# Kernel optimization log

Measured on AMD Instinct MI355X. Metric: run time of the kernel, lower is better.

Reference implementation:

```python
import jax, jax.numpy as jnp
import numpy as np

B, S, D, H, L = 64, 512, 1024, 1024, 2


def setup_inputs() -> dict:
    key = jax.random.key(0)
    ks = jax.random.split(key, 5)
    scale = 1.0 / np.sqrt(D + H)  # ~torch Linear init scale
    return {
        "x": jax.random.normal(ks[0], (B, S, D), dtype=jnp.float32),
        "W_r": jax.random.normal(ks[1], (L, D + H, H), dtype=jnp.float32) * scale,
        "W_z": jax.random.normal(ks[2], (L, D + H, H), dtype=jnp.float32) * scale,
        "W_h": jax.random.normal(ks[3], (L, D + H, H), dtype=jnp.float32) * scale,
        "b_r": jnp.zeros((L, H), dtype=jnp.float32),
        "b_z": jnp.zeros((L, H), dtype=jnp.float32),
        "b_h": jnp.zeros((L, H), dtype=jnp.float32),
    }


def _gru_layer(x_seq, Wr, Wz, Wh, br, bz, bh):
    # x_seq: [S, B, D]; returns [S, B, H]
    h0 = jnp.zeros((x_seq.shape[1], Wr.shape[1]), dtype=x_seq.dtype)

    def step(h, xt):
        xh = jnp.concatenate([xt, h], axis=-1)          # [B, D+H]
        r = jax.nn.sigmoid(xh @ Wr + br)
        z = jax.nn.sigmoid(xh @ Wz + bz)
        xrh = jnp.concatenate([xt, r * h], axis=-1)
        n = jnp.tanh(xrh @ Wh + bh)
        h_new = (1.0 - z) * n + z * h
        return h_new, h_new

    _, ys = jax.lax.scan(step, h0, x_seq)
    return ys


def reference(x, W_r, W_z, W_h, b_r, b_z, b_h):
    seq = jnp.swapaxes(x, 0, 1)  # [S, B, D]
    for i in range(W_r.shape[0]):
        seq = _gru_layer(seq, W_r[i], W_z[i], W_h[i], b_r[i], b_z[i], b_h[i])
    return jnp.swapaxes(seq, 0, 1)  # [B, S, H]
```

## Files before the change

kernel.cpp:

```cpp
#include <hip/hip_runtime.h>


#define TPB 256
#define NBLK 256
#define B_ 64
#define S_ 512
#define H_ 1024
#define KTOT 2048
#define NROW 32768

typedef float f32x4 __attribute__((ext_vector_type(4)));
typedef short short8 __attribute__((ext_vector_type(8)));

#define WX_HI  0
#define WX_LO  12288
#define WRZ_HI 24576
#define WRZ_LO 32768
#define WN_HI  40960
#define WN_LO  45056
#define A_HI   49152
#define A_LO   65536
#define LDS_SHORTS 81920

#define MFMA16 __builtin_amdgcn_mfma_f32_16x16x32_bf16

#define GLL(gp, lp) \
    __builtin_amdgcn_global_load_lds((__attribute__((address_space(1))) const void*)(const void*)(gp), \
                                     (__attribute__((address_space(3))) void*)(void*)(lp), 16, 0, 0x11)

__device__ __forceinline__ unsigned short f2bf(float f) {
    unsigned u = __float_as_uint(f);
    u += 0x7fffu + ((u >> 16) & 1u);
    return (unsigned short)(u >> 16);
}
__device__ __forceinline__ float bf2f(unsigned short s) {
    return __uint_as_float(((unsigned)s) << 16);
}
__device__ __forceinline__ float sigm(float v) { return 1.0f / (1.0f + expf(-v)); }

__device__ __forceinline__ void store_short_bypass(const unsigned short* addr, unsigned short v) {
    asm volatile("global_store_short %0, %1, off sc0 sc1"
                 :: "v"((unsigned long long)(uintptr_t)addr), "v"((unsigned)v) : "memory");
}
__device__ __forceinline__ void waitcnt0() {
    asm volatile("s_waitcnt vmcnt(0)" ::: "memory");
}

__device__ __forceinline__ void gbar(unsigned* bar, int grp) {
    __syncthreads();
    if (threadIdx.x == 0) {
        unsigned* cnt  = bar + grp * 32;
        unsigned* gen  = bar + 256 + grp * 32;
        unsigned* ccnt = bar + 512;
        unsigned g = __hip_atomic_load(gen, __ATOMIC_RELAXED, __HIP_MEMORY_SCOPE_AGENT);
        if (__hip_atomic_fetch_add(cnt, 1u, __ATOMIC_RELAXED, __HIP_MEMORY_SCOPE_AGENT) == 31u) {
            __hip_atomic_store(cnt, 0u, __ATOMIC_RELAXED, __HIP_MEMORY_SCOPE_AGENT);
            waitcnt0();
            if (__hip_atomic_fetch_add(ccnt, 1u, __ATOMIC_RELAXED, __HIP_MEMORY_SCOPE_AGENT) == 7u) {
                __hip_atomic_store(ccnt, 0u, __ATOMIC_RELAXED, __HIP_MEMORY_SCOPE_AGENT);
                waitcnt0();
                #pragma unroll
                for (int i = 0; i < 8; ++i)
                    __hip_atomic_store(bar + 256 + i * 32, g + 1u,
                                       __ATOMIC_RELAXED, __HIP_MEMORY_SCOPE_AGENT);
            } else {
                while (__hip_atomic_load(gen, __ATOMIC_RELAXED, __HIP_MEMORY_SCOPE_AGENT) == g)
                    __builtin_amdgcn_s_sleep(8);
            }
        } else {
            while (__hip_atomic_load(gen, __ATOMIC_RELAXED, __HIP_MEMORY_SCOPE_AGENT) == g)
                __builtin_amdgcn_s_sleep(8);
        }
    }
    __syncthreads();
}

__global__ __launch_bounds__(TPB, 1) void gru_fk(
    const float* __restrict__ x,
    const float* __restrict__ Wr,
    const float* __restrict__ Wz,
    const float* __restrict__ Wh,
    const float* __restrict__ pbr,
    const float* __restrict__ pbz,
    const float* __restrict__ pbh,
    float* __restrict__ out,
    unsigned short* __restrict__ h_hi,
    unsigned short* __restrict__ h_lo,
    unsigned short* __restrict__ rh_hi,
    unsigned short* __restrict__ rh_lo,
    float* __restrict__ hpriv,
    float* __restrict__ zpriv,
    unsigned short* __restrict__ xs_hi,
    unsigned short* __restrict__ xs_lo,
    unsigned* __restrict__ bar)
{
    __shared__ short lds[LDS_SHORTS];
    const int lane = threadIdx.x & 63;
    const int wave = threadIdx.x >> 6;
    const int c0   = blockIdx.x << 2;
    const int grp  = blockIdx.x & 7;
    float* hp = hpriv + (blockIdx.x << 8);
    float* zp = zpriv + (blockIdx.x << 8);

    const int q    = lane >> 4;
    const int jc   = lane & 15;
    const int jcs  = (jc < 12) ? jc : jc - 4;
    const int mrow = wave * 16 + jc;
    const int oct  = q << 3;

    for (int l = 0; l < 2; ++l) {
        if (l == 0) {
            for (int i = threadIdx.x + blockIdx.x * TPB; i < NROW * H_ / 8; i += TPB * NBLK) {
                const float* src = x + (size_t)i * 8;
                float4 v0 = *(const float4*)src;
                float4 v1 = *(const float4*)(src + 4);
                float vv[8] = {v0.x, v0.y, v0.z, v0.w, v1.x, v1.y, v1.z, v1.w};
                short8 hi, lo;
                #pragma unroll
                for (int j = 0; j < 8; ++j) {
                    unsigned short hb = f2bf(vv[j]);
                    hi[j] = (short)hb; lo[j] = (short)f2bf(vv[j] - bf2f(hb));
                }
                *(short8*)&xs_hi[(size_t)i * 8] = hi;
                *(short8*)&xs_lo[(size_t)i * 8] = lo;
            }
            __threadfence();
            waitcnt0();
        }
        gbar(bar, grp);

        for (int g = threadIdx.x; g < 1536; g += TPB) {
            int n = g % 12, ko = g / 12;
            int k = ko * 8;
            int col = c0 + (n & 3);
            int gate = n >> 2;
            const float* Wg = (gate == 0) ? Wr : (gate == 1) ? Wz : Wh;
            short8 hi, lo;
            #pragma unroll
            for (int j = 0; j < 8; ++j) {
                float v = Wg[((size_t)(l * KTOT + k + j)) * H_ + col];
                unsigned short hb = f2bf(v);
                hi[j] = (short)hb; lo[j] = (short)f2bf(v - bf2f(hb));
            }
            *(short8*)&lds[WX_HI + g * 8] = hi;
            *(short8*)&lds[WX_LO + g * 8] = lo;
        }
        for (int g = threadIdx.x; g < 1024; g += TPB) {
            int n = g & 7, ko = g >> 3;
            int k = 1024 + ko * 8;
            int col = c0 + (n & 3);
            const float* Wg = (n < 4) ? Wr : Wz;
            short8 hi, lo;
            #pragma unroll
            for (int j = 0; j < 8; ++j) {
                float v = Wg[((size_t)(l * KTOT + k + j)) * H_ + col];
                unsigned short hb = f2bf(v);
                hi[j] = (short)hb; lo[j] = (short)f2bf(v - bf2f(hb));
            }
            *(short8*)&lds[WRZ_HI + g * 8] = hi;
            *(short8*)&lds[WRZ_LO + g * 8] = lo;
        }
        for (int g = threadIdx.x; g < 512; g += TPB) {
            int n = g & 3, ko = g >> 2;
            int k = 1024 + ko * 8;
            int col = c0 + n;
            short8 hi, lo;
            #pragma unroll
            for (int j = 0; j < 8; ++j) {
                float v = Wh[((size_t)(l * KTOT + k + j)) * H_ + col];
                unsigned short hb = f2bf(v);
                hi[j] = (short)hb; lo[j] = (short)f2bf(v - bf2f(hb));
            }
            *(short8*)&lds[WN_HI + g * 8] = hi;
            *(short8*)&lds[WN_LO + g * 8] = lo;
        }
        {
            int m = threadIdx.x & 63, cc = threadIdx.x >> 6;
            hp[(m << 2) | cc] = 0.0f;
            store_short_bypass(h_hi + m * H_ + c0 + cc, 0);
            store_short_bypass(h_lo + m * H_ + c0 + cc, 0);
        }
        gbar(bar, grp);

        const float brv = pbr[l * H_ + c0 + (jc & 3)];
        const float bzv = pbz[l * H_ + c0 + (jc & 3)];
        const float bhv = pbh[l * H_ + c0 + (jc & 3)];

        for (int t = 0; t < S_; ++t) {
            const size_t xrow = ((size_t)(mrow * S_ + t)) * H_ + oct;
            f32x4 accX = {0.f, 0.f, 0.f, 0.f};
            f32x4 accH = {0.f, 0.f, 0.f, 0.f};

            if (l == 0) {
                for (int c = 0; c < 4; ++c) {
                    #pragma unroll
                    for (int i = 0; i < 8; ++i) {
                        int sg = wave * 8 + i;
                        int kc = sg >> 2, ms = sg & 3;
                        int m  = ms * 16 + (lane & 15);
                        int kh = c * 256 + kc * 32 + ((lane >> 4) << 3);
                        GLL(h_hi + m * H_ + kh, &lds[A_HI + sg * 512]);
                        GLL(h_lo + m * H_ + kh, &lds[A_LO + sg * 512]);
                    }
                    #pragma unroll
                    for (int kk = 0; kk < 8; ++kk) {
                        int ks = c * 8 + kk;
                        short8 ah  = *(const short8*)(xs_hi + xrow + ks * 32);
                        short8 al  = *(const short8*)(xs_lo + xrow + ks * 32);
                        short8 bh_ = *(short8*)&lds[WX_HI + ((ks * 4 + q) * 12 + jcs) * 8];
                        short8 bl_ = *(short8*)&lds[WX_LO + ((ks * 4 + q) * 12 + jcs) * 8];
                        accX = MFMA16(ah, bh_, accX, 0, 0, 0);
                        accX = MFMA16(al, bh_, accX, 0, 0, 0);
                        accX = MFMA16(ah, bl_, accX, 0, 0, 0);
                    }
                    __syncthreads();
                    #pragma unroll
                    for (int kk = 0; kk < 8; ++kk) {
                        int kg = c * 8 + kk;
                        short8 bh_ = *(short8*)&lds[WRZ_HI + ((kg * 4 + q) * 8 + (lane & 7)) * 8];
                        short8 bl_ = *(short8*)&lds[WRZ_LO + ((kg * 4 + q) * 8 + (lane & 7)) * 8];
                        short8 ah  = *(short8*)&lds[A_HI + ((kk * 4 + wave) * 64 + lane) * 8];
                        short8 al  = *(short8*)&lds[A_LO + ((kk * 4 + wave) * 64 + lane) * 8];
                        accH = MFMA16(ah, bh_, accH, 0, 0, 0);
                        accH = MFMA16(al, bh_, accH, 0, 0, 0);
                        accH = MFMA16(ah, bl_, accH, 0, 0, 0);
                    }
                    __syncthreads();
                }
            } else {
                for (int c = 0; c < 4; ++c) {
                    #pragma unroll
                    for (int i = 0; i < 8; ++i) {
                        int sg = wave * 8 + i;
                        int kc = sg >> 2, ms = sg & 3;
                        int m  = ms * 16 + (lane & 15);
                        int kx = c * 256 + kc * 32 + ((lane >> 4) << 3);
                        GLL(xs_hi + ((size_t)(m * S_ + t)) * H_ + kx, &lds[A_HI + sg * 512]);
                        GLL(xs_lo + ((size_t)(m * S_ + t)) * H_ + kx, &lds[A_LO + sg * 512]);
                    }
                    __syncthreads();
                    #pragma unroll
                    for (int kk = 0; kk < 8; ++kk) {
                        int ks = c * 8 + kk;
                        short8 bh_ = *(short8*)&lds[WX_HI + ((ks * 4 + q) * 12 + jcs) * 8];
                        short8 bl_ = *(short8*)&lds[WX_LO + ((ks * 4 + q) * 12 + jcs) * 8];
                        short8 ah  = *(short8*)&lds[A_HI + ((kk * 4 + wave) * 64 + lane) * 8];
                        short8 al  = *(short8*)&lds[A_LO + ((kk * 4 + wave) * 64 + lane) * 8];
                        accX = MFMA16(ah, bh_, accX, 0, 0, 0);
                        accX = MFMA16(al, bh_, accX, 0, 0, 0);
                        accX = MFMA16(ah, bl_, accX, 0, 0, 0);
                    }
                    __syncthreads();
                }
                for (int c = 0; c < 4; ++c) {
                    #pragma unroll
                    for (int i = 0; i < 8; ++i) {
                        int sg = wave * 8 + i;
                        int kc = sg >> 2, ms = sg & 3;
                        int m  = ms * 16 + (lane & 15);
                        int kh = c * 256 + kc * 32 + ((lane >> 4) << 3);
                        GLL(h_hi + m * H_ + kh, &lds[A_HI + sg * 512]);
                        GLL(h_lo + m * H_ + kh, &lds[A_LO + sg * 512]);
                    }
                    __syncthreads();
                    #pragma unroll
                    for (int kk = 0; kk < 8; ++kk) {
                        int kg = c * 8 + kk;
                        short8 bh_ = *(short8*)&lds[WRZ_HI + ((kg * 4 + q) * 8 + (lane & 7)) * 8];
                        short8 bl_ = *(short8*)&lds[WRZ_LO + ((kg * 4 + q) * 8 + (lane & 7)) * 8];
                        short8 ah  = *(short8*)&lds[A_HI + ((kk * 4 + wave) * 64 + lane) * 8];
                        short8 al  = *(short8*)&lds[A_LO + ((kk * 4 + wave) * 64 + lane) * 8];
                        accH = MFMA16(ah, bh_, accH, 0, 0, 0);
                        accH = MFMA16(al, bh_, accH, 0, 0, 0);
                        accH = MFMA16(ah, bl_, accH, 0, 0, 0);
                    }
                    __syncthreads();
                }
            }
            if (jc < 8) {
                const bool isr = jc < 4;
                const int cloc = jc & 3;
                const int col = c0 + cloc;
                const float bias = isr ? brv : bzv;
                #pragma unroll
                for (int i = 0; i < 4; ++i) {
                    int m = wave * 16 + q * 4 + i;
                    float gt = sigm(accX[i] + accH[i] + bias);
                    if (isr) {
                        float rh = gt * hp[(m << 2) | cloc];
                        unsigned short hb2 = f2bf(rh);
                        store_short_bypass(rh_hi + m * H_ + col, hb2);
                        store_short_bypass(rh_lo + m * H_ + col, f2bf(rh - bf2f(hb2)));
                    } else {
                        zp[(m << 2) | cloc] = gt;
                    }
                }
            } else if (l == 0 && jc >= 12 && t > 0) {
                const int cl = jc - 12;
                #pragma unroll
                for (int i = 0; i < 4; ++i) {
                    int m = wave * 16 + q * 4 + i;
                    float hv = hp[(m << 2) | cl];
                    unsigned short hb2 = f2bf(hv);
                    size_t off = ((size_t)(m * S_ + (t - 1))) * H_ + c0 + cl;
                    xs_hi[off] = hb2;
                    xs_lo[off] = f2bf(hv - bf2f(hb2));
                }
            }
            gbar(bar, grp);

            f32x4 acc2 = {0.f, 0.f, 0.f, 0.f};
            for (int c = 0; c < 4; ++c) {
                #pragma unroll
                for (int i = 0; i < 8; ++i) {
                    int sg = wave * 8 + i;
                    int kc = sg >> 2, ms = sg & 3;
                    int m  = ms * 16 + (lane & 15);
                    int kh = c * 256 + kc * 32 + ((lane >> 4) << 3);
                    GLL(rh_hi + m * H_ + kh, &lds[A_HI + sg * 512]);
                    GLL(rh_lo + m * H_ + kh, &lds[A_LO + sg * 512]);
                }
                __syncthreads();
                #pragma unroll
                for (int kk = 0; kk < 8; ++kk) {
                    int kg = c * 8 + kk;
                    short8 bh_ = *(short8*)&lds[WN_HI + ((kg * 4 + q) * 4 + (lane & 3)) * 8];
                    short8 bl_ = *(short8*)&lds[WN_LO + ((kg * 4 + q) * 4 + (lane & 3)) * 8];
                    short8 ah  = *(short8*)&lds[A_HI + ((kk * 4 + wave) * 64 + lane) * 8];
                    short8 al  = *(short8*)&lds[A_LO + ((kk * 4 + wave) * 64 + lane) * 8];
                    acc2 = MFMA16(ah, bh_, acc2, 0, 0, 0);
                    acc2 = MFMA16(al, bh_, acc2, 0, 0, 0);
                    acc2 = MFMA16(ah, bl_, acc2, 0, 0, 0);
                }
                __syncthreads();
            }
            if (jc >= 8 && jc < 12) {
                const int cl = jc & 3;
                const int col = c0 + cl;
                #pragma unroll
                for (int i = 0; i < 4; ++i) {
                    int m = wave * 16 + q * 4 + i;
                    float nv = tanhf(accX[i] + acc2[i] + bhv);
                    float zz = zp[(m << 2) | cl];
                    float ho = hp[(m << 2) | cl];
                    float hn = (1.0f - zz) * nv + zz * ho;
                    hp[(m << 2) | cl] = hn;
                    unsigned short hb2 = f2bf(hn);
                    unsigned short lb2 = f2bf(hn - bf2f(hb2));
                    store_short_bypass(h_hi + m * H_ + col, hb2);
                    store_short_bypass(h_lo + m * H_ + col, lb2);
                    if (l == 1) out[((size_t)(m * S_ + t)) * H_ + col] = hn;
                }
            }
            gbar(bar, grp);
        }

        if (l == 0) {
            if (jc >= 12) {
                const int cl = jc - 12;
                #pragma unroll
                for (int i = 0; i < 4; ++i) {
                    int m = wave * 16 + q * 4 + i;
                    float hv = hp[(m << 2) | cl];
                    unsigned short hb2 = f2bf(hv);
                    size_t off = ((size_t)(m * S_ + 511)) * H_ + c0 + cl;
                    xs_hi[off] = hb2;
                    xs_lo[off] = f2bf(hv - bf2f(hb2));
                }
            }
            __threadfence();
            waitcnt0();
        }
    }
}

extern "C" void kernel_launch(void* const* d_in, const int* in_sizes, int n_in,
                              void* d_out, int out_size, void* d_ws, size_t ws_size,
                              hipStream_t stream) {
    const float* x  = (const float*)d_in[0];
    const float* Wr = (const float*)d_in[1];
    const float* Wz = (const float*)d_in[2];
    const float* Wh = (const float*)d_in[3];
    const float* br = (const float*)d_in[4];
    const float* bz = (const float*)d_in[5];
    const float* bh = (const float*)d_in[6];
    float* out = (float*)d_out;

    char* ws = (char*)d_ws;
    unsigned* bar        = (unsigned*)ws;
    unsigned short* h_hi = (unsigned short*)(ws + 4096);
    unsigned short* h_lo = (unsigned short*)(ws + 135168);
    unsigned short* rhhi = (unsigned short*)(ws + 266240);
    unsigned short* rhlo = (unsigned short*)(ws + 397312);
    float* hpriv         = (float*)(ws + 528384);
    float* zpriv         = (float*)(ws + 790528);
    unsigned short* xshi = (unsigned short*)(ws + (2ull  << 20));
    unsigned short* xslo = (unsigned short*)(ws + (66ull << 20));

    hipMemsetAsync(d_ws, 0, 4096, stream);
    gru_fk<<<NBLK, TPB, 0, stream>>>(x, Wr, Wz, Wh, br, bz, bh, out,
                                     h_hi, h_lo, rhhi, rhlo, hpriv, zpriv,
                                     xshi, xslo, bar);
}
```

Before: 40.25 ms.

## Keep GRU state in registers and unify layer paths with overlapped x-projection

Keeps the per-block hidden state and z gate in registers, exchanged between lanes with shuffles, in place of the global hpriv/zpriv scratch buffers. Layer 1 now uses the same fused step as layer 0, reading x directly from global memory while the h tiles stream into LDS, so the separate x-tile load stage is gone. It also drops the cache-policy bits on global_load_lds, adds an agent-scope acquire fence after each grid barrier, and writes xs and the output with cache-bypassing stores. The added cross-block ordering depends on the new fence and the bypass stores, which risks coherence problems.

```diff
diff --git a/kernel.cpp b/kernel.cpp
--- a/kernel.cpp
+++ b/kernel.cpp
@@ -26,7 +26,7 @@
 
 #define GLL(gp, lp) \
     __builtin_amdgcn_global_load_lds((__attribute__((address_space(1))) const void*)(const void*)(gp), \
-                                     (__attribute__((address_space(3))) void*)(void*)(lp), 16, 0, 0x11)
+                                     (__attribute__((address_space(3))) void*)(void*)(lp), 16, 0, 0)
 
 __device__ __forceinline__ unsigned short f2bf(float f) {
     unsigned u = __float_as_uint(f);
@@ -41,6 +41,10 @@
 __device__ __forceinline__ void store_short_bypass(const unsigned short* addr, unsigned short v) {
     asm volatile("global_store_short %0, %1, off sc0 sc1"
                  :: "v"((unsigned long long)(uintptr_t)addr), "v"((unsigned)v) : "memory");
+}
+__device__ __forceinline__ void store_f32_bypass(const float* addr, float v) {
+    asm volatile("global_store_dword %0, %1, off sc0 sc1"
+                 :: "v"((unsigned long long)(uintptr_t)addr), "v"(v) : "memory");
 }
 __device__ __forceinline__ void waitcnt0() {
     asm volatile("s_waitcnt vmcnt(0)" ::: "memory");
@@ -73,6 +77,7 @@
         }
     }
     __syncthreads();
+    __builtin_amdgcn_fence(__ATOMIC_ACQUIRE, "agent");
 }
 
 __global__ __launch_bounds__(TPB, 1) void gru_fk(
@@ -88,8 +93,6 @@
     unsigned short* __restrict__ h_lo,
     unsigned short* __restrict__ rh_hi,
     unsigned short* __restrict__ rh_lo,
-    float* __restrict__ hpriv,
-    float* __restrict__ zpriv,
     unsigned short* __restrict__ xs_hi,
     unsigned short* __restrict__ xs_lo,
     unsigned* __restrict__ bar)
@@ -99,14 +102,16 @@
     const int wave = threadIdx.x >> 6;
     const int c0   = blockIdx.x << 2;
     const int grp  = blockIdx.x & 7;
-    float* hp = hpriv + (blockIdx.x << 8);
-    float* zp = zpriv + (blockIdx.x << 8);
 
     const int q    = lane >> 4;
     const int jc   = lane & 15;
     const int jcs  = (jc < 12) ? jc : jc - 4;
     const int mrow = wave * 16 + jc;
     const int oct  = q << 3;
+
+    float hreg[4], zreg[4];
+    #pragma unroll
+    for (int i = 0; i < 4; ++i) { hreg[i] = 0.f; zreg[i] = 0.f; }
 
     for (int l = 0; l < 2; ++l) {
         if (l == 0) {
@@ -175,8 +180,9 @@
             *(short8*)&lds[WN_LO + g * 8] = lo;
         }
         {
+            #pragma unroll
+            for (int i = 0; i < 4; ++i) hreg[i] = 0.f;
             int m = threadIdx.x & 63, cc = threadIdx.x >> 6;
-            hp[(m << 2) | cc] = 0.0f;
             store_short_bypass(h_hi + m * H_ + c0 + cc, 0);
             store_short_bypass(h_lo + m * H_ + c0 + cc, 0);
         }
@@ -191,91 +197,46 @@
             f32x4 accX = {0.f, 0.f, 0.f, 0.f};
             f32x4 accH = {0.f, 0.f, 0.f, 0.f};
 
-            if (l == 0) {
-                for (int c = 0; c < 4; ++c) {
-                    #pragma unroll
-                    for (int i = 0; i < 8; ++i) {
-                        int sg = wave * 8 + i;
-                        int kc = sg >> 2, ms = sg & 3;
-                        int m  = ms * 16 + (lane & 15);
-                        int kh = c * 256 + kc * 32 + ((lane >> 4) << 3);
-                        GLL(h_hi + m * H_ + kh, &lds[A_HI + sg * 512]);
-                        GLL(h_lo + m * H_ + kh, &lds[A_LO + sg * 512]);
-                    }
-                    #pragma unroll
-                    for (int kk = 0; kk < 8; ++kk) {
-                        int ks = c * 8 + kk;
-                        short8 ah  = *(const short8*)(xs_hi + xrow + ks * 32);
-                        short8 al  = *(const short8*)(xs_lo + xrow + ks * 32);
-                        short8 bh_ = *(short8*)&lds[WX_HI + ((ks * 4 + q) * 12 + jcs) * 8];
-                        short8 bl_ = *(short8*)&lds[WX_LO + ((ks * 4 + q) * 12 + jcs) * 8];
-                        accX = MFMA16(ah, bh_, accX, 0, 0, 0);
-                        accX = MFMA16(al, bh_, accX, 0, 0, 0);
-                        accX = MFMA16(ah, bl_, accX, 0, 0, 0);
-                    }
-                    __syncthreads();
-                    #pragma unroll
-                    for (int kk = 0; kk < 8; ++kk) {
-                        int kg = c * 8 + kk;
-                        short8 bh_ = *(short8*)&lds[WRZ_HI + ((kg * 4 + q) * 8 + (lane & 7)) * 8];
-                        short8 bl_ = *(short8*)&lds[WRZ_LO + ((kg * 4 + q) * 8 + (lane & 7)) * 8];
-                        short8 ah  = *(short8*)&lds[A_HI + ((kk * 4 + wave) * 64 + lane) * 8];
-                        short8 al  = *(short8*)&lds[A_LO + ((kk * 4 + wave) * 64 + lane) * 8];
-                        accH = MFMA16(ah, bh_, accH, 0, 0, 0);
-                        accH = MFMA16(al, bh_, accH, 0, 0, 0);
-                        accH = MFMA16(ah, bl_, accH, 0, 0, 0);
-                    }
-                    __syncthreads();
-                }
-            } else {
-                for (int c = 0; c < 4; ++c) {
-                    #pragma unroll
-                    for (int i = 0; i < 8; ++i) {
-                        int sg = wave * 8 + i;
-                        int kc = sg >> 2, ms = sg & 3;
-                        int m  = ms * 16 + (lane & 15);
-                        int kx = c * 256 + kc * 32 + ((lane >> 4) << 3);
-                        GLL(xs_hi + ((size_t)(m * S_ + t)) * H_ + kx, &lds[A_HI + sg * 512]);
-                        GLL(xs_lo + ((size_t)(m * S_ + t)) * H_ + kx, &lds[A_LO + sg * 512]);
-                    }
-                    __syncthreads();
-                    #pragma unroll
-                    for (int kk = 0; kk < 8; ++kk) {
-                        int ks = c * 8 + kk;
-                        short8 bh_ = *(short8*)&lds[WX_HI + ((ks * 4 + q) * 12 + jcs) * 8];
-                        short8 bl_ = *(short8*)&lds[WX_LO + ((ks * 4 + q) * 12 + jcs) * 8];
-                        short8 ah  = *(short8*)&lds[A_HI + ((kk * 4 + wave) * 64 + lane) * 8];
-                        short8 al  = *(short8*)&lds[A_LO + ((kk * 4 + wave) * 64 + lane) * 8];
-                        accX = MFMA16(ah, bh_, accX, 0, 0, 0);
-                        accX = MFMA16(al, bh_, accX, 0, 0, 0);
-                        accX = MFMA16(ah, bl_, accX, 0, 0, 0);
-                    }
-                    __syncthreads();
-                }
-                for (int c = 0; c < 4; ++c) {
-                    #pragma unroll
-                    for (int i = 0; i < 8; ++i) {
-                        int sg = wave * 8 + i;
-                        int kc = sg >> 2, ms = sg & 3;
-                        int m  = ms * 16 + (lane & 15);
-                        int kh = c * 256 + kc * 32 + ((lane >> 4) << 3);
-                        GLL(h_hi + m * H_ + kh, &lds[A_HI + sg * 512]);
-                        GLL(h_lo + m * H_ + kh, &lds[A_LO + sg * 512]);
-                    }
-                    __syncthreads();
-                    #pragma unroll
-                    for (int kk = 0; kk < 8; ++kk) {
-                        int kg = c * 8 + kk;
-                        short8 bh_ = *(short8*)&lds[WRZ_HI + ((kg * 4 + q) * 8 + (lane & 7)) * 8];
-                        short8 bl_ = *(short8*)&lds[WRZ_LO + ((kg * 4 + q) * 8 + (lane & 7)) * 8];
-                        short8 ah  = *(short8*)&lds[A_HI + ((kk * 4 + wave) * 64 + lane) * 8];
-                        short8 al  = *(short8*)&lds[A_LO + ((kk * 4 + wave) * 64 + lane) * 8];
-                        accH = MFMA16(ah, bh_, accH, 0, 0, 0);
-                        accH = MFMA16(al, bh_, accH, 0, 0, 0);
-                        accH = MFMA16(ah, bl_, accH, 0, 0, 0);
-                    }
-                    __syncthreads();
-                }
+            for (int c = 0; c < 4; ++c) {
+                #pragma unroll
+                for (int i = 0; i < 8; ++i) {
+                    int sg = wave * 8 + i;
+                    int kc = sg >> 2, ms = sg & 3;
+                    int m  = ms * 16 + (lane & 15);
+                    int kh = c * 256 + kc * 32 + ((lane >> 4) << 3);
+                    GLL(h_hi + m * H_ + kh, &lds[A_HI + sg * 512]);
+                    GLL(h_lo + m * H_ + kh, &lds[A_LO + sg * 512]);
+                }
+                #pragma unroll
+                for (int kk = 0; kk < 8; ++kk) {
+                    int ks = c * 8 + kk;
+                    short8 ah  = *(const short8*)(xs_hi + xrow + ks * 32);
+                    short8 al  = *(const short8*)(xs_lo + xrow + ks * 32);
+                    short8 bh_ = *(short8*)&lds[WX_HI + ((ks * 4 + q) * 12 + jcs) * 8];
+                    short8 bl_ = *(short8*)&lds[WX_LO + ((ks * 4 + q) * 12 + jcs) * 8];
+                    accX = MFMA16(ah, bh_, accX, 0, 0, 0);
+                    accX = MFMA16(al, bh_, accX, 0, 0, 0);
+                    accX = MFMA16(ah, bl_, accX, 0, 0, 0);
+                }
+                __syncthreads();
+                #pragma unroll
+                for (int kk = 0; kk < 8; ++kk) {
+                    int kg = c * 8 + kk;
+                    short8 bh_ = *(short8*)&lds[WRZ_HI + ((kg * 4 + q) * 8 + (lane & 7)) * 8];
+                    short8 bl_ = *(short8*)&lds[WRZ_LO + ((kg * 4 + q) * 8 + (lane & 7)) * 8];
+                    short8 ah  = *(short8*)&lds[A_HI + ((kk * 4 + wave) * 64 + lane) * 8];
+                    short8 al  = *(short8*)&lds[A_LO + ((kk * 4 + wave) * 64 + lane) * 8];
+                    accH = MFMA16(ah, bh_, accH, 0, 0, 0);
+                    accH = MFMA16(al, bh_, accH, 0, 0, 0);
+                    accH = MFMA16(ah, bl_, accH, 0, 0, 0);
+                }
+                __syncthreads();
+            }
+            float hA[4], hRW[4];
+            #pragma unroll
+            for (int i = 0; i < 4; ++i) {
+                hA[i]  = __shfl(hreg[i], (lane + 8) & 63, 64);
+                hRW[i] = __shfl(hreg[i], (lane + 60) & 63, 64);
             }
             if (jc < 8) {
                 const bool isr = jc < 4;
@@ -287,12 +248,12 @@
                     int m = wave * 16 + q * 4 + i;
                     float gt = sigm(accX[i] + accH[i] + bias);
                     if (isr) {
-                        float rh = gt * hp[(m << 2) | cloc];
+                        float rh = gt * hA[i];
                         unsigned short hb2 = f2bf(rh);
                         store_short_bypass(rh_hi + m * H_ + col, hb2);
                         store_short_bypass(rh_lo + m * H_ + col, f2bf(rh - bf2f(hb2)));
                     } else {
-                        zp[(m << 2) | cloc] = gt;
+                        zreg[i] = gt;
                     }
                 }
             } else if (l == 0 && jc >= 12 && t > 0) {
@@ -300,11 +261,11 @@
                 #pragma unroll
                 for (int i = 0; i < 4; ++i) {
                     int m = wave * 16 + q * 4 + i;
-                    float hv = hp[(m << 2) | cl];
+                    float hv = hRW[i];
                     unsigned short hb2 = f2bf(hv);
                     size_t off = ((size_t)(m * S_ + (t - 1))) * H_ + c0 + cl;
-                    xs_hi[off] = hb2;
-                    xs_lo[off] = f2bf(hv - bf2f(hb2));
+                    store_short_bypass(xs_hi + off, hb2);
+                    store_short_bypass(xs_lo + off, f2bf(hv - bf2f(hb2)));
                 }
             }
             gbar(bar, grp);
@@ -334,6 +295,10 @@
                 }
                 __syncthreads();
             }
+            float zzv[4];
+            #pragma unroll
+            for (int i = 0; i < 4; ++i)
+                zzv[i] = __shfl(zreg[i], (lane + 60) & 63, 64);
             if (jc >= 8 && jc < 12) {
                 const int cl = jc & 3;
                 const int col = c0 + cl;
@@ -341,35 +306,37 @@
                 for (int i = 0; i < 4; ++i) {
                     int m = wave * 16 + q * 4 + i;
                     float nv = tanhf(accX[i] + acc2[i] + bhv);
-                    float zz = zp[(m << 2) | cl];
-                    float ho = hp[(m << 2) | cl];
+                    float zz = zzv[i];
+                    float ho = hreg[i];
                     float hn = (1.0f - zz) * nv + zz * ho;
-                    hp[(m << 2) | cl] = hn;
+                    hreg[i] = hn;
                     unsigned short hb2 = f2bf(hn);
                     unsigned short lb2 = f2bf(hn - bf2f(hb2));
                     store_short_bypass(h_hi + m * H_ + col, hb2);
                     store_short_bypass(h_lo + m * H_ + col, lb2);
-                    if (l == 1) out[((size_t)(m * S_ + t)) * H_ + col] = hn;
+                    if (l == 1) store_f32_bypass(out + ((size_t)(m * S_ + t)) * H_ + col, hn);
                 }
             }
             gbar(bar, grp);
         }
 
         if (l == 0) {
+            float hF[4];
+            #pragma unroll
+            for (int i = 0; i < 4; ++i)
+                hF[i] = __shfl(hreg[i], (lane + 60) & 63, 64);
             if (jc >= 12) {
                 const int cl = jc - 12;
                 #pragma unroll
                 for (int i = 0; i < 4; ++i) {
                     int m = wave * 16 + q * 4 + i;
-                    float hv = hp[(m << 2) | cl];
+                    float hv = hF[i];
                     unsigned short hb2 = f2bf(hv);
                     size_t off = ((size_t)(m * S_ + 511)) * H_ + c0 + cl;
-                    xs_hi[off] = hb2;
-                    xs_lo[off] = f2bf(hv - bf2f(hb2));
-                }
-            }
-            __threadfence();
-            waitcnt0();
+                    store_short_bypass(xs_hi + off, hb2);
+                    store_short_bypass(xs_lo + off, f2bf(hv - bf2f(hb2)));
+                }
+            }
         }
     }
 }
@@ -392,13 +359,11 @@
     unsigned short* h_lo = (unsigned short*)(ws + 135168);
     unsigned short* rhhi = (unsigned short*)(ws + 266240);
     unsigned short* rhlo = (unsigned short*)(ws + 397312);
-    float* hpriv         = (float*)(ws + 528384);
-    float* zpriv         = (float*)(ws + 790528);
     unsigned short* xshi = (unsigned short*)(ws + (2ull  << 20));
     unsigned short* xslo = (unsigned short*)(ws + (66ull << 20));
 
     hipMemsetAsync(d_ws, 0, 4096, stream);
     gru_fk<<<NBLK, TPB, 0, stream>>>(x, Wr, Wz, Wh, br, bz, bh, out,
-                                     h_hi, h_lo, rhhi, rhlo, hpriv, zpriv,
+                                     h_hi, h_lo, rhhi, rhlo,
                                      xshi, xslo, bar);
 }
```

Result: slower. 50.37 ms (+25.1%).
